# Kernel tuning notes

Measured on AMD Instinct MI355X. Metric: run time of the kernel, lower is better.

Reference implementation:

```python
import jax, jax.numpy as jnp
import numpy as np

B, S, HID = 4, 2048, 576
NH, NKV, HD = 9, 3, 64
MAXPOS, THETA = 8192, 100000.0


def rotate_half(x):
    x1, x2 = x[..., : x.shape[-1] // 2], x[..., x.shape[-1] // 2 :]
    return jnp.concatenate((-x2, x1), axis=-1)


def setup_inputs() -> dict:
    key = jax.random.key(0)
    ks = jax.random.split(key, 6)
    x = jax.random.normal(ks[0], (B, S, HID), dtype=jnp.float32)
    # RoPE tables (HuggingFace layout: freqs duplicated across halves)
    inv_freq = 1.0 / (THETA ** (np.arange(0, HD, 2, dtype=np.float32) / HD))
    freqs = np.outer(np.arange(MAXPOS, dtype=np.float32), inv_freq)
    emb = np.concatenate([freqs, freqs], axis=-1)
    cos = jnp.asarray(np.cos(emb))
    sin = jnp.asarray(np.sin(emb))
    position_ids = jnp.broadcast_to(jnp.arange(S, dtype=jnp.int64), (B, S))
    # additive causal mask [B,1,S,S]
    causal = jnp.where(
        jnp.tril(jnp.ones((S, S), dtype=bool)), 0.0, -1e9
    ).astype(jnp.float32)
    attention_mask = jnp.broadcast_to(causal, (B, 1, S, S))
    scale = 0.02
    wq = jax.random.normal(ks[1], (NH * HD, HID), dtype=jnp.float32) * scale
    wk = jax.random.normal(ks[2], (NKV * HD, HID), dtype=jnp.float32) * scale
    wv = jax.random.normal(ks[3], (NKV * HD, HID), dtype=jnp.float32) * scale
    wo = jax.random.normal(ks[4], (HID, NH * HD), dtype=jnp.float32) * scale
    return {
        "x": x, "cos": cos, "sin": sin, "position_ids": position_ids,
        "attention_mask": attention_mask,
        "wq": wq, "wk": wk, "wv": wv, "wo": wo,
    }


def reference(x, cos, sin, position_ids, attention_mask, wq, wk, wv, wo):
    b, s, _ = x.shape
    # projections (nn.Linear: y = x @ W.T), split into heads -> [B,H,S,D]
    q = (x @ wq.T).reshape(b, s, NH, HD).transpose(0, 2, 1, 3)
    k = (x @ wk.T).reshape(b, s, NKV, HD).transpose(0, 2, 1, 3)
    v = (x @ wv.T).reshape(b, s, NKV, HD).transpose(0, 2, 1, 3)
    # RoPE: cos/sin gathered per position -> [B,1,S,D], broadcast over heads
    c = cos[position_ids][:, None, :, :]
    si = sin[position_ids][:, None, :, :]
    q = q * c + rotate_half(q) * si
    k = k * c + rotate_half(k) * si
    # GQA expansion: repeat_interleave kv heads to match q heads
    k = jnp.repeat(k, NH // NKV, axis=1)
    v = jnp.repeat(v, NH // NKV, axis=1)
    scale = 1.0 / jnp.sqrt(jnp.asarray(HD, dtype=x.dtype))
    scores = jnp.einsum("bhqd,bhkd->bhqk", q, k) * scale + attention_mask
    attn = jax.nn.softmax(scores.astype(jnp.float32), axis=-1).astype(q.dtype)
    out = jnp.einsum("bhqk,bhkd->bhqd", attn, v)
    out = out.transpose(0, 2, 1, 3).reshape(b, s, NH * HD)
    return out @ wo.T
```

## Files before the change

kernel.cpp:

```cpp
#include <hip/hip_runtime.h>
#include <hip/hip_bf16.h>

#define B_    4
#define S_    2048
#define HID_  576
#define NH_   9
#define NKV_  3
#define HD_   64
#define GQ_   3

typedef __attribute__((ext_vector_type(8))) short bf16x8;
typedef __attribute__((ext_vector_type(4))) float f32x4;

__device__ __forceinline__ short f2bf(float f) {
    union { float f; unsigned int u; } v; v.f = f;
    unsigned int r = (v.u + 0x7fffu + ((v.u >> 16) & 1u)) >> 16;
    return (short)r;
}

__device__ __forceinline__ unsigned int cvt_pk_bf16(float a, float b) {
    unsigned int r;
    asm("v_cvt_pk_bf16_f32 %0, %1, %2" : "=v"(r) : "v"(a), "v"(b));
    return r;
}

__device__ __forceinline__ float exp2fast(float x) {
    return __builtin_amdgcn_exp2f(x);
}

__device__ __forceinline__ void async16(const void* g, void* l) {
    __builtin_amdgcn_global_load_lds(
        (const __attribute__((address_space(1))) unsigned int*)g,
        (__attribute__((address_space(3))) unsigned int*)l, 16, 0, 0);
}

#define NX_   (8192 * 576)
#define NWQ_  (576 * 576)
#define NWK_  (192 * 576)
#define NWV_  (192 * 576)
#define NWO_  (576 * 576)
#define NTOT_ (NX_ + NWQ_ + NWK_ + NWV_ + NWO_)

__global__ __launch_bounds__(256) void convert_kernel(
    const float* __restrict__ x,  const float* __restrict__ wq,
    const float* __restrict__ wk, const float* __restrict__ wv,
    const float* __restrict__ wo,
    short* __restrict__ xb, short* __restrict__ wqkvb, short* __restrict__ wob)
{
    int i4 = (blockIdx.x * 256 + threadIdx.x) * 4;
    const float* src; short* dst;
    if (i4 < NX_)                          { src = x  + i4;                          dst = xb    + i4; }
    else if (i4 < NX_ + NWQ_)              { src = wq + (i4 - NX_);                  dst = wqkvb + (i4 - NX_); }
    else if (i4 < NX_ + NWQ_ + NWK_)       { src = wk + (i4 - NX_ - NWQ_);           dst = wqkvb + (i4 - NX_); }
    else if (i4 < NX_ + NWQ_ + NWK_ + NWV_){ src = wv + (i4 - NX_ - NWQ_ - NWK_);    dst = wqkvb + (i4 - NX_); }
    else                                   { src = wo + (i4 - NX_ - NWQ_ - NWK_ - NWV_);
                                             dst = wob + (i4 - NX_ - NWQ_ - NWK_ - NWV_); }
    float4 v = *(const float4*)src;
    short4 o = make_short4(f2bf(v.x), f2bf(v.y), f2bf(v.z), f2bf(v.w));
    *(short4*)dst = o;
}

__global__ __launch_bounds__(256) void qkv_kernel(
    const short* __restrict__ xb,
    const short* __restrict__ wqkvb,
    const float* __restrict__ cosb,
    const float* __restrict__ sinb,
    short* __restrict__ Q,
    short* __restrict__ K,
    short* __restrict__ Vt)
{
    __shared__ __align__(16) short As[2][256 * 64];
    __shared__ __align__(16) short Bs[2][64 * 64];

    const int bid = blockIdx.x;
    const int f   = (bid & 7) * 60 + (bid >> 3);
    const int m0     = (f / 15) * 256;
    const int nb_blk = f % 15;
    const int tid  = threadIdx.x;
    const int w    = tid >> 6, lane = tid & 63;
    const int quad = lane >> 4, c = lane & 15;
    const int lr   = lane >> 3, lg = lane & 7;
    const int sw   = lg ^ lr;
    const int xg   = quad ^ (c & 7);

    auto stage = [&](int step, short* dstA, short* dstB) {
        const int k0 = step * 64;
        #pragma unroll
        for (int r = 0; r < 8; ++r) {
            int ch = w * 8 + r, R = ch * 8 + lr;
            async16(xb + (size_t)(m0 + R) * HID_ + k0 + sw * 8, (char*)dstA + ch * 1024);
        }
        #pragma unroll
        for (int r = 0; r < 2; ++r) {
            int ch = w * 2 + r, R = ch * 8 + lr;
            async16(wqkvb + (size_t)(nb_blk * 64 + R) * HID_ + k0 + sw * 8, (char*)dstB + ch * 1024);
        }
    };

    f32x4 acc[4][4];
    #pragma unroll
    for (int mt = 0; mt < 4; ++mt)
        #pragma unroll
        for (int nb = 0; nb < 4; ++nb) acc[mt][nb] = (f32x4){0.f, 0.f, 0.f, 0.f};

    stage(0, As[0], Bs[0]);

    int buf = 0;
    for (int kk = 0; kk < 9; ++kk) {
        __syncthreads();
        if (kk < 8) stage(kk + 1, As[buf ^ 1], Bs[buf ^ 1]);

        const short* a_s = As[buf];
        const short* b_s = Bs[buf];
        bf16x8 bfr[4][2];
        #pragma unroll
        for (int nb = 0; nb < 4; ++nb) {
            int row = nb * 16 + c;
            bfr[nb][0] = *(const bf16x8*)(b_s + row * 64 + xg * 8);
            bfr[nb][1] = *(const bf16x8*)(b_s + row * 64 + (xg ^ 4) * 8);
        }
        #pragma unroll
        for (int mt = 0; mt < 4; ++mt) {
            int row = w * 64 + mt * 16 + c;
            bf16x8 a0 = *(const bf16x8*)(a_s + row * 64 + xg * 8);
            bf16x8 a1 = *(const bf16x8*)(a_s + row * 64 + (xg ^ 4) * 8);
            #pragma unroll
            for (int nb = 0; nb < 4; ++nb) {
                acc[mt][nb] = __builtin_amdgcn_mfma_f32_16x16x32_bf16(a0, bfr[nb][0], acc[mt][nb], 0, 0, 0);
                acc[mt][nb] = __builtin_amdgcn_mfma_f32_16x16x32_bf16(a1, bfr[nb][1], acc[mt][nb], 0, 0, 0);
            }
        }
        buf ^= 1;
    }

    int type, head;
    if (nb_blk < NH_)            { type = 0; head = nb_blk; }
    else if (nb_blk < NH_ + NKV_){ type = 1; head = nb_blk - NH_; }
    else                         { type = 2; head = nb_blk - NH_ - NKV_; }
    const int b  = m0 >> 11;
    const int s0 = m0 & (S_ - 1);

    if (type < 2) {
        const float qs = (type == 0) ? 0.18033688f : 1.0f;
        #pragma unroll
        for (int mt = 0; mt < 4; ++mt)
            #pragma unroll
            for (int reg = 0; reg < 4; ++reg) {
                int s = s0 + w * 64 + mt * 16 + quad * 4 + reg;
                const float* cr = cosb + (size_t)s * HD_;
                const float* sr = sinb + (size_t)s * HD_;
                float a0 = acc[mt][0][reg], a1 = acc[mt][1][reg];
                float a2 = acc[mt][2][reg], a3 = acc[mt][3][reg];
                float o0 = (a0 * cr[c]      - a2 * sr[c])      * qs;
                float o1 = (a1 * cr[c + 16] - a3 * sr[c + 16]) * qs;
                float o2 = (a2 * cr[c + 32] + a0 * sr[c + 32]) * qs;
                float o3 = (a3 * cr[c + 48] + a1 * sr[c + 48]) * qs;
                short* dst = (type == 0)
                    ? Q + (((size_t)b * NH_  + head) * S_ + s) * HD_
                    : K + (((size_t)b * NKV_ + head) * S_ + s) * HD_;
                dst[c]      = f2bf(o0);
                dst[c + 16] = f2bf(o1);
                dst[c + 32] = f2bf(o2);
                dst[c + 48] = f2bf(o3);
            }
    } else {
        short* base = Vt + (((size_t)b * NKV_ + head) * HD_) * S_;
        #pragma unroll
        for (int mt = 0; mt < 4; ++mt) {
            int s4 = s0 + w * 64 + mt * 16 + quad * 4;
            #pragma unroll
            for (int nb = 0; nb < 4; ++nb) {
                int d = nb * 16 + c;
                short4 pk = make_short4(f2bf(acc[mt][nb][0]), f2bf(acc[mt][nb][1]),
                                        f2bf(acc[mt][nb][2]), f2bf(acc[mt][nb][3]));
                *(short4*)(base + (size_t)d * S_ + s4) = pk;
            }
        }
    }
}

#define PSH 40

__global__ __launch_bounds__(256) void attn_kernel(
    const short* __restrict__ Q,
    const short* __restrict__ K,
    const short* __restrict__ Vt,
    short* __restrict__ AOb)
{
    __shared__ __align__(16) short Ks[2][64 * 64];
    __shared__ __align__(16) short Vs[2][64 * 64];
    __shared__ __align__(16) short Ps[64 * PSH];

    const int hb = blockIdx.x;
    const int h  = hb >> 2, b = hb & 3;
    const int qt = 31 - blockIdx.y;
    const int kh = h / GQ_;
    const int tid  = threadIdx.x;
    const int w    = tid >> 6, lane = tid & 63;
    const int quad = lane >> 4, c = lane & 15;
    const int lr   = lane >> 3, lg = lane & 7;
    const int sw   = lg ^ lr;
    const int xg   = quad ^ (c & 7);

    const short* Qg = Q  + (((size_t)b * NH_  + h ) * S_ + qt * 64) * HD_;
    const short* Kg = K  + (((size_t)b * NKV_ + kh) * S_) * HD_;
    const short* Vg = Vt + (((size_t)b * NKV_ + kh) * HD_) * S_;

    bf16x8 aq0 = *(const bf16x8*)(Qg + (w * 16 + c) * HD_ + quad * 8);
    bf16x8 aq1 = *(const bf16x8*)(Qg + (w * 16 + c) * HD_ + 32 + quad * 8);

    const bool stK = (w < 2);
    const int  ch0 = (w & 1) * 4;
    const short* gs[4];
    #pragma unroll
    for (int r = 0; r < 4; ++r) {
        int ch = ch0 + r;
        gs[r] = stK ? Kg + (size_t)(ch * 8 + lr) * HD_ + sw * 8
                    : Vg + (size_t)(ch * 8 + lr) * S_  + sw * 8;
    }
    const int gstep = stK ? 64 * HD_ : 64;

    #pragma unroll
    for (int r = 0; r < 4; ++r)
        async16(gs[r], (char*)(stK ? Ks[0] : Vs[0]) + (ch0 + r) * 1024);

    bf16x8 ones;
    #pragma unroll
    for (int i = 0; i < 8; ++i) ones[i] = (short)0x3F80;

    f32x4 acc_o[4];
    #pragma unroll
    for (int nb = 0; nb < 4; ++nb) acc_o[nb] = (f32x4){0.f, 0.f, 0.f, 0.f};
    f32x4 acc_l = (f32x4){0.f, 0.f, 0.f, 0.f};

    auto do_tile = [&](const short* ks, const short* vs, bool MASK) {
        f32x4 sc[4];
        #pragma unroll
        for (int nb = 0; nb < 4; ++nb) {
            bf16x8 bk0 = *(const bf16x8*)(ks + (nb * 16 + c) * 64 + xg * 8);
            bf16x8 bk1 = *(const bf16x8*)(ks + (nb * 16 + c) * 64 + (xg ^ 4) * 8);
            f32x4 z = (f32x4){0.f, 0.f, 0.f, 0.f};
            z = __builtin_amdgcn_mfma_f32_16x16x32_bf16(bk0, aq0, z, 0, 0, 0);
            z = __builtin_amdgcn_mfma_f32_16x16x32_bf16(bk1, aq1, z, 0, 0, 0);
            sc[nb] = z;
        }
        #pragma unroll
        for (int ph = 0; ph < 2; ++ph) {
            #pragma unroll
            for (int nbh = 0; nbh < 2; ++nbh) {
                const int nb = ph * 2 + nbh;
                float p[4];
                #pragma unroll
                for (int r = 0; r < 4; ++r) {
                    float pv = exp2fast(sc[nb][r] - 4.0f);
                    if (MASK && (nb * 16 + quad * 4 + r > w * 16 + c)) pv = 0.f;
                    p[r] = pv;
                }
                uint2 t;
                t.x = cvt_pk_bf16(p[0], p[1]);
                t.y = cvt_pk_bf16(p[2], p[3]);
                *(uint2*)(Ps + (w * 16 + c) * PSH + nbh * 16 + quad * 4) = t;
            }
            bf16x8 ap = *(const bf16x8*)(Ps + (w * 16 + c) * PSH + quad * 8);
            const int pg = ph ? (xg ^ 4) : xg;
            #pragma unroll
            for (int nb2 = 0; nb2 < 4; ++nb2) {
                bf16x8 bv = *(const bf16x8*)(vs + (nb2 * 16 + c) * 64 + pg * 8);
                acc_o[nb2] = __builtin_amdgcn_mfma_f32_16x16x32_bf16(ap, bv, acc_o[nb2], 0, 0, 0);
            }
            acc_l = __builtin_amdgcn_mfma_f32_16x16x32_bf16(ap, ones, acc_l, 0, 0, 0);
        }
    };

    __syncthreads();
    int buf = 0;
    for (int kt = 0; kt < qt; ++kt) {
        int nxt = buf ^ 1;
        #pragma unroll
        for (int r = 0; r < 4; ++r) {
            gs[r] += gstep;
            async16(gs[r], (char*)(stK ? Ks[nxt] : Vs[nxt]) + (ch0 + r) * 1024);
        }
        do_tile(Ks[buf], Vs[buf], false);
        __syncthreads();
        buf ^= 1;
    }
    do_tile(Ks[buf], Vs[buf], true);

    #pragma unroll
    for (int r = 0; r < 4; ++r) {
        int s = qt * 64 + w * 16 + quad * 4 + r;
        float inv = 1.f / acc_l[r];
        short* dst = AOb + (((size_t)b * S_ + s) * NH_ + h) * HD_;
        #pragma unroll
        for (int nb = 0; nb < 4; ++nb)
            dst[nb * 16 + c] = f2bf(acc_o[nb][r] * inv);
    }
}

__global__ __launch_bounds__(256) void oproj_kernel(
    const short* __restrict__ AOb,
    const short* __restrict__ wob,
    float* __restrict__ out)
{
    __shared__ __align__(16) short As[2][256 * 64];
    __shared__ __align__(16) short Bs[2][64 * 64];

    const int bid = blockIdx.x;
    const int f   = (bid & 7) * 36 + (bid >> 3);
    const int m0 = (f / 9) * 256;
    const int n0 = (f % 9) * 64;
    const int tid  = threadIdx.x;
    const int w    = tid >> 6, lane = tid & 63;
    const int quad = lane >> 4, c = lane & 15;
    const int lr   = lane >> 3, lg = lane & 7;
    const int sw   = lg ^ lr;
    const int xg   = quad ^ (c & 7);

    auto stage = [&](int step, short* dstA, short* dstB) {
        const int k0 = step * 64;
        #pragma unroll
        for (int r = 0; r < 8; ++r) {
            int ch = w * 8 + r, R = ch * 8 + lr;
            async16(AOb + (size_t)(m0 + R) * HID_ + k0 + sw * 8, (char*)dstA + ch * 1024);
        }
        #pragma unroll
        for (int r = 0; r < 2; ++r) {
            int ch = w * 2 + r, R = ch * 8 + lr;
            async16(wob + (size_t)(n0 + R) * HID_ + k0 + sw * 8, (char*)dstB + ch * 1024);
        }
    };

    f32x4 acc[4][4];
    #pragma unroll
    for (int mt = 0; mt < 4; ++mt)
        #pragma unroll
        for (int nb = 0; nb < 4; ++nb) acc[mt][nb] = (f32x4){0.f, 0.f, 0.f, 0.f};

    stage(0, As[0], Bs[0]);

    int buf = 0;
    for (int kk = 0; kk < 9; ++kk) {
        __syncthreads();
        if (kk < 8) stage(kk + 1, As[buf ^ 1], Bs[buf ^ 1]);

        const short* a_s = As[buf];
        const short* b_s = Bs[buf];
        bf16x8 bfr[4][2];
        #pragma unroll
        for (int nb = 0; nb < 4; ++nb) {
            int row = nb * 16 + c;
            bfr[nb][0] = *(const bf16x8*)(b_s + row * 64 + xg * 8);
            bfr[nb][1] = *(const bf16x8*)(b_s + row * 64 + (xg ^ 4) * 8);
        }
        #pragma unroll
        for (int mt = 0; mt < 4; ++mt) {
            int row = w * 64 + mt * 16 + c;
            bf16x8 a0 = *(const bf16x8*)(a_s + row * 64 + xg * 8);
            bf16x8 a1 = *(const bf16x8*)(a_s + row * 64 + (xg ^ 4) * 8);
            #pragma unroll
            for (int nb = 0; nb < 4; ++nb) {
                acc[mt][nb] = __builtin_amdgcn_mfma_f32_16x16x32_bf16(a0, bfr[nb][0], acc[mt][nb], 0, 0, 0);
                acc[mt][nb] = __builtin_amdgcn_mfma_f32_16x16x32_bf16(a1, bfr[nb][1], acc[mt][nb], 0, 0, 0);
            }
        }
        buf ^= 1;
    }

    #pragma unroll
    for (int mt = 0; mt < 4; ++mt)
        #pragma unroll
        for (int reg = 0; reg < 4; ++reg) {
            int m = m0 + w * 64 + mt * 16 + quad * 4 + reg;
            float* dst = out + (size_t)m * HID_ + n0;
            #pragma unroll
            for (int nb = 0; nb < 4; ++nb)
                dst[nb * 16 + c] = acc[mt][nb][reg];
        }
}

extern "C" void kernel_launch(void* const* d_in, const int* in_sizes, int n_in,
                              void* d_out, int out_size, void* d_ws, size_t ws_size,
                              hipStream_t stream) {
    const float* x    = (const float*)d_in[0];
    const float* cosb = (const float*)d_in[1];
    const float* sinb = (const float*)d_in[2];
    const float* wq   = (const float*)d_in[5];
    const float* wk   = (const float*)d_in[6];
    const float* wv   = (const float*)d_in[7];
    const float* wo   = (const float*)d_in[8];

    short* xb    = (short*)d_ws;
    short* wqkvb = xb    + (size_t)NX_;
    short* wob   = wqkvb + (size_t)(NWQ_ + NWK_ + NWV_);
    short* Qb    = wob   + (size_t)NWO_;
    short* Kb    = Qb    + (size_t)B_ * NH_  * S_ * HD_;
    short* Vtb   = Kb    + (size_t)B_ * NKV_ * S_ * HD_;
    short* AOb   = Vtb   + (size_t)B_ * NKV_ * S_ * HD_;

    convert_kernel<<<dim3(NTOT_ / 4 / 256), dim3(256), 0, stream>>>(
        x, wq, wk, wv, wo, xb, wqkvb, wob);
    qkv_kernel<<<dim3(480), dim3(256), 0, stream>>>(
        xb, wqkvb, cosb, sinb, Qb, Kb, Vtb);
    attn_kernel<<<dim3(36, 32), dim3(256), 0, stream>>>(Qb, Kb, Vtb, AOb);
    oproj_kernel<<<dim3(288), dim3(256), 0, stream>>>(AOb, wob, (float*)d_out);
}
```

Before: 192.7 us.

## Switch attention to 32x32x16 MFMA with split-KV waves and register-resident P

Rewrites the attention inner loop to use 32x32x16 bf16 MFMAs. Each wave now owns 32 query rows and one half of the 64-key tile, and the two KV halves are merged through shared memory at the end. The probability tile is repacked in registers with v_permlane32_swap instead of a round trip through shared memory. The row-sum now comes from a scalar add plus a shuffle instead of an MFMA against a ones vector. This aims to cut LDS traffic and MFMA instruction count, but adds a final cross-wave reduction and leaves one wave idle on the diagonal tile.

After: 186.3 us. 3.3% less time.

```diff
diff --git a/kernel.cpp b/kernel.cpp
--- a/kernel.cpp
+++ b/kernel.cpp
@@ -11,6 +11,7 @@
 
 typedef __attribute__((ext_vector_type(8))) short bf16x8;
 typedef __attribute__((ext_vector_type(4))) float f32x4;
+typedef __attribute__((ext_vector_type(16))) float f32x16;
 
 __device__ __forceinline__ short f2bf(float f) {
     union { float f; unsigned int u; } v; v.f = f;
@@ -179,17 +180,15 @@
     }
 }
 
-#define PSH 40
-
 __global__ __launch_bounds__(256) void attn_kernel(
     const short* __restrict__ Q,
     const short* __restrict__ K,
     const short* __restrict__ Vt,
     short* __restrict__ AOb)
 {
-    __shared__ __align__(16) short Ks[2][64 * 64];
-    __shared__ __align__(16) short Vs[2][64 * 64];
-    __shared__ __align__(16) short Ps[64 * PSH];
+    __shared__ __align__(16) char smem[32768];
+    short* KsB = (short*)smem;
+    short* VsB = (short*)(smem + 16384);
 
     const int hb = blockIdx.x;
     const int h  = hb >> 2, b = hb & 3;
@@ -197,17 +196,19 @@
     const int kh = h / GQ_;
     const int tid  = threadIdx.x;
     const int w    = tid >> 6, lane = tid & 63;
-    const int quad = lane >> 4, c = lane & 15;
+    const int l31  = lane & 31, hi = lane >> 5, l7 = lane & 7;
     const int lr   = lane >> 3, lg = lane & 7;
     const int sw   = lg ^ lr;
-    const int xg   = quad ^ (c & 7);
+    const int qh   = w >> 1, kv = w & 1;
 
     const short* Qg = Q  + (((size_t)b * NH_  + h ) * S_ + qt * 64) * HD_;
     const short* Kg = K  + (((size_t)b * NKV_ + kh) * S_) * HD_;
     const short* Vg = Vt + (((size_t)b * NKV_ + kh) * HD_) * S_;
 
-    bf16x8 aq0 = *(const bf16x8*)(Qg + (w * 16 + c) * HD_ + quad * 8);
-    bf16x8 aq1 = *(const bf16x8*)(Qg + (w * 16 + c) * HD_ + 32 + quad * 8);
+    bf16x8 aq[4];
+    #pragma unroll
+    for (int ks = 0; ks < 4; ++ks)
+        aq[ks] = *(const bf16x8*)(Qg + (size_t)(qh * 32 + l31) * HD_ + (2 * ks + hi) * 8);
 
     const bool stK = (w < 2);
     const int  ch0 = (w & 1) * 4;
@@ -222,79 +223,100 @@
 
     #pragma unroll
     for (int r = 0; r < 4; ++r)
-        async16(gs[r], (char*)(stK ? Ks[0] : Vs[0]) + (ch0 + r) * 1024);
-
-    bf16x8 ones;
-    #pragma unroll
-    for (int i = 0; i < 8; ++i) ones[i] = (short)0x3F80;
-
-    f32x4 acc_o[4];
-    #pragma unroll
-    for (int nb = 0; nb < 4; ++nb) acc_o[nb] = (f32x4){0.f, 0.f, 0.f, 0.f};
-    f32x4 acc_l = (f32x4){0.f, 0.f, 0.f, 0.f};
-
-    auto do_tile = [&](const short* ks, const short* vs, bool MASK) {
-        f32x4 sc[4];
-        #pragma unroll
-        for (int nb = 0; nb < 4; ++nb) {
-            bf16x8 bk0 = *(const bf16x8*)(ks + (nb * 16 + c) * 64 + xg * 8);
-            bf16x8 bk1 = *(const bf16x8*)(ks + (nb * 16 + c) * 64 + (xg ^ 4) * 8);
-            f32x4 z = (f32x4){0.f, 0.f, 0.f, 0.f};
-            z = __builtin_amdgcn_mfma_f32_16x16x32_bf16(bk0, aq0, z, 0, 0, 0);
-            z = __builtin_amdgcn_mfma_f32_16x16x32_bf16(bk1, aq1, z, 0, 0, 0);
-            sc[nb] = z;
-        }
-        #pragma unroll
-        for (int ph = 0; ph < 2; ++ph) {
-            #pragma unroll
-            for (int nbh = 0; nbh < 2; ++nbh) {
-                const int nb = ph * 2 + nbh;
-                float p[4];
-                #pragma unroll
-                for (int r = 0; r < 4; ++r) {
-                    float pv = exp2fast(sc[nb][r] - 4.0f);
-                    if (MASK && (nb * 16 + quad * 4 + r > w * 16 + c)) pv = 0.f;
-                    p[r] = pv;
-                }
-                uint2 t;
-                t.x = cvt_pk_bf16(p[0], p[1]);
-                t.y = cvt_pk_bf16(p[2], p[3]);
-                *(uint2*)(Ps + (w * 16 + c) * PSH + nbh * 16 + quad * 4) = t;
-            }
-            bf16x8 ap = *(const bf16x8*)(Ps + (w * 16 + c) * PSH + quad * 8);
-            const int pg = ph ? (xg ^ 4) : xg;
-            #pragma unroll
-            for (int nb2 = 0; nb2 < 4; ++nb2) {
-                bf16x8 bv = *(const bf16x8*)(vs + (nb2 * 16 + c) * 64 + pg * 8);
-                acc_o[nb2] = __builtin_amdgcn_mfma_f32_16x16x32_bf16(ap, bv, acc_o[nb2], 0, 0, 0);
-            }
-            acc_l = __builtin_amdgcn_mfma_f32_16x16x32_bf16(ap, ones, acc_l, 0, 0, 0);
+        async16(gs[r], (char*)(stK ? KsB : VsB) + (ch0 + r) * 1024);
+
+    f32x16 acc_o[2];
+    #pragma unroll
+    for (int dt = 0; dt < 2; ++dt)
+        #pragma unroll
+        for (int i = 0; i < 16; ++i) acc_o[dt][i] = 0.f;
+    float acc_ls = 0.f;
+
+    auto do_tile = [&](const short* ksb, const short* vsb, bool MASK) {
+        if (MASK && kv > qh) return;
+        f32x16 z;
+        #pragma unroll
+        for (int i = 0; i < 16; ++i) z[i] = 0.f;
+        #pragma unroll
+        for (int ks = 0; ks < 4; ++ks) {
+            bf16x8 ak = *(const bf16x8*)(ksb + (kv * 32 + l31) * 64 + ((2 * ks + hi) ^ l7) * 8);
+            z = __builtin_amdgcn_mfma_f32_32x32x16_bf16(ak, aq[ks], z, 0, 0, 0);
+        }
+        float p[16];
+        #pragma unroll
+        for (int r = 0; r < 16; ++r) {
+            float pv = exp2fast(z[r] - 4.0f);
+            if (MASK && kv == qh && ((r & 3) + 8 * (r >> 2) + 4 * hi > l31)) pv = 0.f;
+            p[r] = pv;
+        }
+        float lp = 0.f;
+        #pragma unroll
+        for (int r = 0; r < 16; ++r) lp += p[r];
+        acc_ls += lp;
+        #pragma unroll
+        for (int k2 = 0; k2 < 2; ++k2) {
+            unsigned int u0 = cvt_pk_bf16(p[k2 * 8 + 0], p[k2 * 8 + 1]);
+            unsigned int u1 = cvt_pk_bf16(p[k2 * 8 + 2], p[k2 * 8 + 3]);
+            unsigned int v0 = cvt_pk_bf16(p[k2 * 8 + 4], p[k2 * 8 + 5]);
+            unsigned int v1 = cvt_pk_bf16(p[k2 * 8 + 6], p[k2 * 8 + 7]);
+            asm("v_permlane32_swap_b32 %0, %1" : "+v"(u0), "+v"(v0));
+            asm("v_permlane32_swap_b32 %0, %1" : "+v"(u1), "+v"(v1));
+            union { unsigned int u[4]; bf16x8 v8; } af;
+            af.u[0] = u0; af.u[1] = u1; af.u[2] = v0; af.u[3] = v1;
+            #pragma unroll
+            for (int dt = 0; dt < 2; ++dt) {
+                bf16x8 bv = *(const bf16x8*)(vsb + (dt * 32 + l31) * 64 + ((kv * 4 + k2 * 2 + hi) ^ l7) * 8);
+                acc_o[dt] = __builtin_amdgcn_mfma_f32_32x32x16_bf16(af.v8, bv, acc_o[dt], 0, 0, 0);
+            }
         }
     };
 
     __syncthreads();
     int buf = 0;
     for (int kt = 0; kt < qt; ++kt) {
-        int nxt = buf ^ 1;
         #pragma unroll
         for (int r = 0; r < 4; ++r) {
             gs[r] += gstep;
-            async16(gs[r], (char*)(stK ? Ks[nxt] : Vs[nxt]) + (ch0 + r) * 1024);
-        }
-        do_tile(Ks[buf], Vs[buf], false);
+            async16(gs[r], (char*)(stK ? KsB : VsB) + (buf ^ 1) * 8192 + (ch0 + r) * 1024);
+        }
+        do_tile(KsB + buf * 4096, VsB + buf * 4096, false);
         __syncthreads();
         buf ^= 1;
     }
-    do_tile(Ks[buf], Vs[buf], true);
-
-    #pragma unroll
-    for (int r = 0; r < 4; ++r) {
-        int s = qt * 64 + w * 16 + quad * 4 + r;
-        float inv = 1.f / acc_l[r];
-        short* dst = AOb + (((size_t)b * S_ + s) * NH_ + h) * HD_;
-        #pragma unroll
-        for (int nb = 0; nb < 4; ++nb)
-            dst[nb * 16 + c] = f2bf(acc_o[nb][r] * inv);
+    do_tile(KsB + buf * 4096, VsB + buf * 4096, true);
+
+    float ls2 = acc_ls + __shfl_xor(acc_ls, 32);
+    float* sc  = (float*)smem;
+    float* scl = sc + 4096;
+    __syncthreads();
+    if (kv == 1) {
+        #pragma unroll
+        for (int dt = 0; dt < 2; ++dt)
+            #pragma unroll
+            for (int r = 0; r < 16; ++r)
+                sc[qh * 2048 + (dt * 16 + r) * 64 + lane] = acc_o[dt][r];
+        if (lane < 32) scl[qh * 32 + lane] = ls2;
+    }
+    __syncthreads();
+    if (kv == 0) {
+        #pragma unroll
+        for (int dt = 0; dt < 2; ++dt)
+            #pragma unroll
+            for (int r = 0; r < 16; ++r)
+                acc_o[dt][r] += sc[qh * 2048 + (dt * 16 + r) * 64 + lane];
+        float lt = ls2 + scl[qh * 32 + l31];
+        float linv = 1.0f / lt;
+        if (lane < 32) scl[qh * 32 + lane] = linv;
+        #pragma unroll
+        for (int dt = 0; dt < 2; ++dt)
+            #pragma unroll
+            for (int r = 0; r < 16; ++r) {
+                int q = (r & 3) + 8 * (r >> 2) + 4 * hi;
+                int s = qt * 64 + qh * 32 + q;
+                float li = scl[qh * 32 + q];
+                AOb[(((size_t)b * S_ + s) * NH_ + h) * HD_ + dt * 32 + l31] =
+                    f2bf(acc_o[dt][r] * li);
+            }
     }
 }
 
```
